# Kernel tuning notes

Hardware: AMD Instinct MI355X
Metric: run time of the kernel (lower is better)

## Reference

```python
import jax, jax.numpy as jnp
import numpy as np

B, T, C = 4, 2048, 1024
H = 16
HD = C // H  # 64
OBS_DIM, ACT_DIM = 17, 6
JOINED_DIM = OBS_DIM + ACT_DIM + 2  # 25


def _make_mask():
    # tril causal mask with every (JOINED_DIM-1 + k*JOINED_DIM)-th column zeroed (RL branch)
    m = np.tril(np.ones((T, T), dtype=np.float32))
    m[:, JOINED_DIM - 1::JOINED_DIM] = 0.0
    return jnp.asarray(m > 0)  # bool [T, T]


MASK = _make_mask()


def setup_inputs() -> dict:
    key = jax.random.key(0)
    ks = jax.random.split(key, 9)
    s = 1.0 / np.sqrt(C)
    return {
        "x": jax.random.normal(ks[0], (B, T, C), dtype=jnp.float32),
        "Wq": jax.random.normal(ks[1], (C, C), dtype=jnp.float32) * s,
        "bq": jax.random.normal(ks[2], (C,), dtype=jnp.float32) * s,
        "Wk": jax.random.normal(ks[3], (C, C), dtype=jnp.float32) * s,
        "bk": jax.random.normal(ks[4], (C,), dtype=jnp.float32) * s,
        "Wv": jax.random.normal(ks[5], (C, C), dtype=jnp.float32) * s,
        "bv": jax.random.normal(ks[6], (C,), dtype=jnp.float32) * s,
        "Wp": jax.random.normal(ks[7], (C, C), dtype=jnp.float32) * s,
        "bp": jax.random.normal(ks[8], (C,), dtype=jnp.float32) * s,
    }


def reference(x, Wq, bq, Wk, bk, Wv, bv, Wp, bp):
    # torch nn.Linear: y = x @ W.T + b
    def split_heads(t):  # [B,T,C] -> [B,H,T,HD]
        return t.reshape(B, T, H, HD).transpose(0, 2, 1, 3)

    q = split_heads(x @ Wq.T + bq)
    k = split_heads(x @ Wk.T + bk)
    v = split_heads(x @ Wv.T + bv)

    att = jnp.einsum("bhqd,bhkd->bhqk", q, k) * (1.0 / np.sqrt(HD))
    att = jnp.where(MASK[None, None, :, :], att, -jnp.inf)
    att = jax.nn.softmax(att, axis=-1)
    # dropout layers are identity in eval mode

    y = jnp.einsum("bhqk,bhkd->bhqd", att, v)  # [B,H,T,HD]
    y = y.transpose(0, 2, 1, 3).reshape(B, T, C)
    return y @ Wp.T + bp
```

## Files before the change

kernel.cpp:

```cpp
#include <hip/hip_runtime.h>
#include <hip/hip_bf16.h>


typedef __attribute__((ext_vector_type(8))) short short8;
typedef __attribute__((ext_vector_type(4))) short short4v;
typedef __attribute__((ext_vector_type(4))) float floatx4;
typedef unsigned short us;

__device__ __forceinline__ us f2bf(float f){
    union { __hip_bfloat16 h; us u; } cv;
    cv.h = __float2bfloat16(f);
    return cv.u;
}

__device__ __forceinline__ void ld_g2l16(const void* g, void* l){
    __builtin_amdgcn_global_load_lds((const __attribute__((address_space(1))) void*)g,
                                     (__attribute__((address_space(3))) void*)l, 16, 0, 0);
}

__global__ __launch_bounds__(256) void cvt_kernel(const float* __restrict__ in,
                                                  us* __restrict__ out, int n4){
    int i = blockIdx.x * 256 + threadIdx.x;
    if (i < n4){
        float4 v = reinterpret_cast<const float4*>(in)[i];
        ushort4 o;
        o.x = f2bf(v.x); o.y = f2bf(v.y); o.z = f2bf(v.z); o.w = f2bf(v.w);
        reinterpret_cast<ushort4*>(out)[i] = o;
    }
}

__global__ __launch_bounds__(256) void cvt4_kernel(const float* __restrict__ w0, const float* __restrict__ w1,
                                                   const float* __restrict__ w2, const float* __restrict__ w3,
                                                   us* __restrict__ o0, us* __restrict__ o1,
                                                   us* __restrict__ o2, us* __restrict__ o3){
    int wsel = blockIdx.x >> 10;
    int i = (blockIdx.x & 1023) * 256 + threadIdx.x;
    const float* src = (wsel == 0) ? w0 : (wsel == 1) ? w1 : (wsel == 2) ? w2 : w3;
    us* dst = (wsel == 0) ? o0 : (wsel == 1) ? o1 : (wsel == 2) ? o2 : o3;
    float4 v = reinterpret_cast<const float4*>(src)[i];
    ushort4 o;
    o.x = f2bf(v.x); o.y = f2bf(v.y); o.z = f2bf(v.z); o.w = f2bf(v.w);
    reinterpret_cast<ushort4*>(dst)[i] = o;
}


#define QSCALE 0.1803368801111244f

#define BAR() __builtin_amdgcn_s_barrier()
#define SGB0() __builtin_amdgcn_sched_barrier(0)
#define LGKM0() do { asm volatile("s_waitcnt lgkmcnt(0)" ::: "memory"); __builtin_amdgcn_sched_barrier(0); } while(0)
#define VMC6() asm volatile("s_waitcnt vmcnt(6)" ::: "memory")
#define VMC4() asm volatile("s_waitcnt vmcnt(4)" ::: "memory")
#define VMC0() asm volatile("s_waitcnt vmcnt(0)" ::: "memory")

#define STAGE_A3(buf, kt) do { \
    _Pragma("unroll") \
    for (int c_ = 0; c_ < 4; c_++) \
        ld_g2l16(Ag + (size_t)(m0 + srow[c_])*1024 + (kt)*64 + sgr[c_]*8, \
                 &smem[(buf)*24576 + (c_*8 + wave)*512]); \
} while(0)

#define STAGE_B3(buf, kt) do { \
    _Pragma("unroll") \
    for (int c_ = 0; c_ < 2; c_++) \
        ld_g2l16(Wb + (size_t)(n0 + srow[c_])*1024 + (kt)*64 + sgr[c_]*8, \
                 &smem[(buf)*24576 + 16384 + (c_*8 + wave)*512]); \
} while(0)

#define LOAD_SET3(buf, KS, AF, BF) do { \
    _Pragma("unroll") \
    for (int i_ = 0; i_ < 4; i_++){ \
        int ra_ = wmm*64 + i_*16 + lane15; \
        int ga_ = ((KS)*4 + quad) ^ (ra_ & 7); \
        AF[i_] = *reinterpret_cast<const short8*>(&smem[(buf)*24576 + ra_*64 + ga_*8]); \
    } \
    _Pragma("unroll") \
    for (int j_ = 0; j_ < 4; j_++){ \
        int rb_ = wnn*64 + j_*16 + lane15; \
        int gb_ = ((KS)*4 + quad) ^ (rb_ & 7); \
        BF[j_] = *reinterpret_cast<const short8*>(&smem[(buf)*24576 + 16384 + rb_*64 + gb_*8]); \
    } \
} while(0)

#define MFMA_SET3(AF, BF) do { \
    __builtin_amdgcn_s_setprio(1); \
    _Pragma("unroll") \
    for (int i_ = 0; i_ < 4; i_++) \
        _Pragma("unroll") \
        for (int j_ = 0; j_ < 4; j_++) \
            acc[i_][j_] = __builtin_amdgcn_mfma_f32_16x16x32_bf16( \
                AF[i_], BF[j_], acc[i_][j_], 0, 0, 0); \
    __builtin_amdgcn_s_setprio(0); \
} while(0)

#define KLOOP3() do { \
    STAGE_A3(0, 0); STAGE_B3(0, 0); \
    STAGE_A3(1, 1); STAGE_B3(1, 1); \
    VMC6(); BAR(); \
    LOAD_SET3(0, 0, afE, bfE); LGKM0(); \
    _Pragma("unroll") \
    for (int t = 0; t < 16; t++){ \
        const int cur = t % 3, nxt = (t + 2) % 3, nx1 = (t + 1) % 3; \
         \
        LOAD_SET3(cur, 1, afO, bfO); \
        SGB0(); \
        if (t < 14) STAGE_A3(nxt, t + 2); \
        MFMA_SET3(afE, bfE); \
        LGKM0(); \
        if (t < 14) { VMC4(); } else if (t == 14) { VMC0(); } \
        BAR(); \
         \
        if (t < 15){ LOAD_SET3(nx1, 0, afE, bfE); SGB0(); } \
        if (t < 14) STAGE_B3(nxt, t + 2); \
        MFMA_SET3(afO, bfO); \
        LGKM0(); \
        BAR(); \
    } \
} while(0)

__global__ __launch_bounds__(512, 2) void gemm_qkv3(
    const us* __restrict__ Ag,
    const us* __restrict__ Wqb, const us* __restrict__ Wkb, const us* __restrict__ Wvb,
    const float* __restrict__ bq, const float* __restrict__ bk, const float* __restrict__ bv,
    us* __restrict__ qo, us* __restrict__ ko, us* __restrict__ vto)
{
    __shared__ us smem[73728];
    const int tid = threadIdx.x;
    const int lane = tid & 63;
    const int wave = tid >> 6;
    const int lane15 = lane & 15;
    const int quad = lane >> 4;
    const int wmm = wave & 3;
    const int wnn = wave >> 2;
    const int seg = blockIdx.x >> 3;
    const int n0 = (blockIdx.x & 7) * 128;
    const int m0 = blockIdx.y * 256;

    const us* Wb = (seg == 0) ? Wqb : (seg == 1) ? Wkb : Wvb;
    const float* bias = (seg == 0) ? bq : (seg == 1) ? bk : bv;

    int srow[4], sgr[4];
    #pragma unroll
    for (int c = 0; c < 4; c++){
        int s = (c*8 + wave)*64 + lane;
        srow[c] = s >> 3;
        sgr[c] = (s & 7) ^ ((s >> 3) & 7);
    }

    floatx4 zero = {0.f, 0.f, 0.f, 0.f};
    floatx4 acc[4][4];
    #pragma unroll
    for (int i = 0; i < 4; i++)
        #pragma unroll
        for (int j = 0; j < 4; j++) acc[i][j] = zero;
    short8 afE[4], bfE[4], afO[4], bfO[4];

    KLOOP3();

    if (seg < 2){
        #pragma unroll
        for (int i = 0; i < 4; i++){
            #pragma unroll
            for (int j = 0; j < 4; j++){
                int n = n0 + wnn*64 + j*16 + lane15;
                float bvv = bias[n];
                #pragma unroll
                for (int r = 0; r < 4; r++){
                    int m = m0 + wmm*64 + i*16 + quad*4 + r;
                    float val = acc[i][j][r] + bvv;
                    if (seg == 0){
                        qo[(size_t)m*1024 + n] = f2bf(val * QSCALE);
                    } else {
                        int b = m >> 11, tt = m & 2047;
                        int h = n >> 6,  d = n & 63;
                        ko[(((size_t)b*16 + h)*2048 + tt)*64 + d] = f2bf(val);
                    }
                }
            }
        }
    } else {
        us* lCT = smem;
        const int b = m0 >> 11;
        const int t0 = m0 & 2047;
        #pragma unroll
        for (int j = 0; j < 4; j++){
            int nl = wnn*64 + j*16 + lane15;
            float bvv = bias[n0 + nl];
            #pragma unroll
            for (int i = 0; i < 4; i++){
                int ml = wmm*64 + i*16 + quad*4;
                unsigned int lo = (unsigned int)f2bf(acc[i][j][0] + bvv) |
                                  ((unsigned int)f2bf(acc[i][j][1] + bvv) << 16);
                unsigned int hi = (unsigned int)f2bf(acc[i][j][2] + bvv) |
                                  ((unsigned int)f2bf(acc[i][j][3] + bvv) << 16);
                uint2 pk2; pk2.x = lo; pk2.y = hi;
                *reinterpret_cast<uint2*>(&lCT[(size_t)nl*264 + ml]) = pk2;
            }
        }
        __syncthreads();
        int nl = tid >> 2;
        int c4 = tid & 3;
        int nC = n0 + nl;
        int h = nC >> 6, d = nC & 63;
        us* dst = vto + (((size_t)b*16 + h)*64 + d)*2048 + t0 + c4*64;
        int rr = (t0 + c4*64) % 25;
        #pragma unroll
        for (int ii = 0; ii < 8; ii++){
            uint4 v = *reinterpret_cast<const uint4*>(&lCT[(size_t)nl*264 + c4*64 + ii*8]);
            us* pv = reinterpret_cast<us*>(&v);
            #pragma unroll
            for (int e = 0; e < 8; e++){
                if (rr == 24) pv[e] = 0;
                rr = (rr == 24) ? 0 : rr + 1;
            }
            *reinterpret_cast<uint4*>(dst + ii*8) = v;
        }
    }
}

__device__ __forceinline__ short8 rdP(const us* pw, int lane15, int ks, int quad){
    const us* a = &pw[lane15*68 + ks*32 + quad*8];
    short4v lo = *reinterpret_cast<const short4v*>(a);
    short4v hi = *reinterpret_cast<const short4v*>(a + 4);
    short8 r = {lo[0], lo[1], lo[2], lo[3], hi[0], hi[1], hi[2], hi[3]};
    return r;
}

__device__ __forceinline__ void pstore_plain(floatx4 (&s)[4], us* pw, int lane15, int quad){
    #pragma unroll
    for (int tj = 0; tj < 4; tj++)
        #pragma unroll
        for (int r = 0; r < 4; r++)
            pw[(quad*4 + r)*68 + tj*16 + lane15] = f2bf(__builtin_amdgcn_exp2f(s[tj][r]));
}

__device__ __forceinline__ void pstore_diag(floatx4 (&s)[4], us* pw, int rgrow, int j0,
                                            int lane15, int quad){
    #pragma unroll
    for (int tj = 0; tj < 4; tj++){
        #pragma unroll
        for (int r = 0; r < 4; r++){
            float p = __builtin_amdgcn_exp2f(s[tj][r]);
            bool kill = (j0 + tj*16 + lane15) > (rgrow + quad*4 + r);
            pw[(quad*4 + r)*68 + tj*16 + lane15] = f2bf(kill ? 0.f : p);
        }
    }
}

#define ATT_STAGE(itn) do { \
    _Pragma("unroll") \
    for (int i_ = 0; i_ < 2; i_++){ \
        ld_g2l16(kb + (size_t)((itn)*64 + srow[i_])*64 + sgr[i_]*8, &lK[(itn) & 1][(i_*4 + wave)*512]); \
        ld_g2l16(vb + (size_t)srow[i_]*2048 + (itn)*64 + sgr[i_]*8, &lV[(itn) & 1][(i_*4 + wave)*512]); \
    } } while(0)

#define ATT_BODY(MODE, ITV) do { \
    const int j0_ = (ITV)*64; \
    __syncthreads(); \
    if ((ITV) + 1 < nIter) ATT_STAGE((ITV) + 1); \
    const us* Kb = lK[(ITV) & 1]; \
    const us* Vb = lV[(ITV) & 1]; \
    floatx4 s0[4], s1[4]; \
    __builtin_amdgcn_s_setprio(1); \
    _Pragma("unroll") \
    for (int tj = 0; tj < 4; tj++){ \
        int rk = tj*16 + lane15; \
        short8 kf0 = *reinterpret_cast<const short8*>(&Kb[rk*64 + ((quad     ^ (rk & 7)))*8]); \
        short8 kf1 = *reinterpret_cast<const short8*>(&Kb[rk*64 + (((4+quad) ^ (rk & 7)))*8]); \
        floatx4 z1 = __builtin_amdgcn_mfma_f32_16x16x32_bf16(qf1a, kf0, zero, 0, 0, 0); \
        s1[tj]     = __builtin_amdgcn_mfma_f32_16x16x32_bf16(qf1b, kf1, z1,   0, 0, 0); \
        if ((MODE) != 2){ \
            floatx4 z0 = __builtin_amdgcn_mfma_f32_16x16x32_bf16(qf0a, kf0, zero, 0, 0, 0); \
            s0[tj]     = __builtin_amdgcn_mfma_f32_16x16x32_bf16(qf0b, kf1, z0,   0, 0, 0); \
        } \
    } \
    __builtin_amdgcn_s_setprio(0); \
    if ((MODE) == 2)      pstore_diag(s1, pw1, rg1, j0_, lane15, quad); \
    else                  pstore_plain(s1, pw1, lane15, quad); \
    if ((MODE) == 1)      pstore_diag(s0, pw0, rg0, j0_, lane15, quad); \
    else if ((MODE) == 0) pstore_plain(s0, pw0, lane15, quad); \
    __builtin_amdgcn_s_setprio(1); \
    _Pragma("unroll") \
    for (int ks = 0; ks < 2; ks++){ \
        short8 mfr = *reinterpret_cast<const short8*>(&lmask[j0_ + ks*32 + quad*8]); \
        short8 pf1 = rdP(pw1, lane15, ks, quad); \
        short8 pf0; \
        lacc1 = __builtin_amdgcn_mfma_f32_16x16x32_bf16(pf1, mfr, lacc1, 0, 0, 0); \
        if ((MODE) != 2){ \
            pf0 = rdP(pw0, lane15, ks, quad); \
            lacc0 = __builtin_amdgcn_mfma_f32_16x16x32_bf16(pf0, mfr, lacc0, 0, 0, 0); \
        } \
        _Pragma("unroll") \
        for (int dt = 0; dt < 4; dt++){ \
            int rv = dt*16 + lane15; \
            short8 vf = *reinterpret_cast<const short8*>(&Vb[rv*64 + (((ks*4+quad) ^ (rv & 7)))*8]); \
            acc1[dt] = __builtin_amdgcn_mfma_f32_16x16x32_bf16(pf1, vf, acc1[dt], 0, 0, 0); \
            if ((MODE) != 2) acc0[dt] = __builtin_amdgcn_mfma_f32_16x16x32_bf16(pf0, vf, acc0[dt], 0, 0, 0); \
        } \
    } \
    __builtin_amdgcn_s_setprio(0); \
} while(0)

__global__ __launch_bounds__(256, 3) void flash_attn(
    const us* __restrict__ q,
    const us* __restrict__ k,
    const us* __restrict__ vT,
    us* __restrict__ y)
{
    __shared__ us lK[2][64*64];
    __shared__ us lV[2][64*64];
    __shared__ us lP[4][2][16*68];
    __shared__ us lmask[2048];
    const int tid = threadIdx.x;
    const int lane = tid & 63;
    const int wave = tid >> 6;
    const int lane15 = lane & 15;
    const int quad = lane >> 4;
    const int lin = blockIdx.x;
    const int qt2 = 15 - (lin >> 6);
    const int bh = lin & 63;
    const int b = bh >> 4, h = bh & 15;
    const int rg0 = qt2*128 + wave*16;
    const int rg1 = rg0 + 64;
    const int nIter = 2*qt2 + 2;

    const us* kb = k  + (size_t)bh*2048*64;
    const us* vb = vT + (size_t)bh*64*2048;

    {
        int c0 = tid * 8;
        int rr = c0 % 25;
        ushort4 mv[2];
        us* pm = reinterpret_cast<us*>(mv);
        #pragma unroll
        for (int e = 0; e < 8; e++){
            pm[e] = (rr == 24) ? (us)0 : (us)0x3F80;
            rr = (rr == 24) ? 0 : rr + 1;
        }
        *reinterpret_cast<uint4*>(&lmask[c0]) = *reinterpret_cast<uint4*>(mv);
    }

    floatx4 zero = {0.f, 0.f, 0.f, 0.f};
    us* pw0 = &lP[wave][0][0];
    us* pw1 = &lP[wave][1][0];

    int srow[2], sgr[2];
    #pragma unroll
    for (int i = 0; i < 2; i++){
        int s = (i*4 + wave)*64 + lane;
        srow[i] = s >> 3;
        sgr[i] = (s & 7) ^ ((s >> 3) & 7);
    }

    const us* q0 = q + ((size_t)b*2048 + rg0 + lane15)*1024 + h*64 + quad*8;
    const us* q1 = q + ((size_t)b*2048 + rg1 + lane15)*1024 + h*64 + quad*8;
    short8 qf0a = *reinterpret_cast<const short8*>(q0);
    short8 qf0b = *reinterpret_cast<const short8*>(q0 + 32);
    short8 qf1a = *reinterpret_cast<const short8*>(q1);
    short8 qf1b = *reinterpret_cast<const short8*>(q1 + 32);

    floatx4 acc0[4], acc1[4];
    #pragma unroll
    for (int d = 0; d < 4; d++){ acc0[d] = zero; acc1[d] = zero; }
    floatx4 lacc0 = zero, lacc1 = zero;

    ATT_STAGE(0);

    int it = 0;
    #pragma unroll 1
    for (; it < nIter - 2; it++) ATT_BODY(0, it);
    ATT_BODY(1, it); it++;
    ATT_BODY(2, it);

    float rl0[4], rl1[4];
    #pragma unroll
    for (int r = 0; r < 4; r++){ rl0[r] = 1.0f / lacc0[r]; rl1[r] = 1.0f / lacc1[r]; }
    #pragma unroll
    for (int dt = 0; dt < 4; dt++){
        #pragma unroll
        for (int r = 0; r < 4; r++){
            int t0 = rg0 + quad*4 + r;
            int t1 = rg1 + quad*4 + r;
            int cc = h*64 + dt*16 + lane15;
            y[((size_t)b*2048 + t0)*1024 + cc] = f2bf(acc0[dt][r] * rl0[r]);
            y[((size_t)b*2048 + t1)*1024 + cc] = f2bf(acc1[dt][r] * rl1[r]);
        }
    }
}

__global__ __launch_bounds__(512, 2) void gemm_out3(
    const us* __restrict__ Ag,
    const us* __restrict__ Wb,
    const float* __restrict__ bias,
    float* __restrict__ out)
{
    __shared__ us smem[73728];
    const int tid = threadIdx.x;
    const int lane = tid & 63;
    const int wave = tid >> 6;
    const int lane15 = lane & 15;
    const int quad = lane >> 4;
    const int wmm = wave & 3;
    const int wnn = wave >> 2;
    const int n0 = blockIdx.x * 128;
    const int m0 = blockIdx.y * 256;

    int srow[4], sgr[4];
    #pragma unroll
    for (int c = 0; c < 4; c++){
        int s = (c*8 + wave)*64 + lane;
        srow[c] = s >> 3;
        sgr[c] = (s & 7) ^ ((s >> 3) & 7);
    }

    floatx4 zero = {0.f, 0.f, 0.f, 0.f};
    floatx4 acc[4][4];
    #pragma unroll
    for (int i = 0; i < 4; i++)
        #pragma unroll
        for (int j = 0; j < 4; j++) acc[i][j] = zero;
    short8 afE[4], bfE[4], afO[4], bfO[4];

    KLOOP3();

    #pragma unroll
    for (int i = 0; i < 4; i++){
        #pragma unroll
        for (int j = 0; j < 4; j++){
            int n = n0 + wnn*64 + j*16 + lane15;
            float bvv = bias[n];
            #pragma unroll
            for (int r = 0; r < 4; r++){
                int m = m0 + wmm*64 + i*16 + quad*4 + r;
                out[(size_t)m*1024 + n] = acc[i][j][r] + bvv;
            }
        }
    }
}

extern "C" void kernel_launch(void* const* d_in, const int* in_sizes, int n_in,
                              void* d_out, int out_size, void* d_ws, size_t ws_size,
                              hipStream_t stream)
{
    const float* x  = (const float*)d_in[0];
    const float* Wq = (const float*)d_in[1];
    const float* bq = (const float*)d_in[2];
    const float* Wk = (const float*)d_in[3];
    const float* bk = (const float*)d_in[4];
    const float* Wv = (const float*)d_in[5];
    const float* bv = (const float*)d_in[6];
    const float* Wp = (const float*)d_in[7];
    const float* bp = (const float*)d_in[8];
    float* out = (float*)d_out;

    us* ws  = (us*)d_ws;
    us* xbf = ws;
    us* wqb = xbf + (size_t)8192*1024;
    us* wkb = wqb + (size_t)1024*1024;
    us* wvb = wkb + (size_t)1024*1024;
    us* wpb = wvb + (size_t)1024*1024;
    us* qws = wpb + (size_t)1024*1024;
    us* kws = qws + (size_t)8388608;
    us* vtw = kws + (size_t)8388608;
    us* yws = vtw + (size_t)8388608;

    cvt_kernel<<<8192, 256, 0, stream>>>(x, xbf, 2097152);
    cvt4_kernel<<<4096, 256, 0, stream>>>(Wq, Wk, Wv, Wp, wqb, wkb, wvb, wpb);

    gemm_qkv3<<<dim3(24, 32), 512, 0, stream>>>(xbf, wqb, wkb, wvb, bq, bk, bv, qws, kws, vtw);

    flash_attn<<<1024, 256, 0, stream>>>(qws, kws, vtw, yws);

    gemm_out3<<<dim3(8, 32), 512, 0, stream>>>(yws, wpb, bp, out);
}
```

Baseline: 256.4 us.

## Enlarge GEMM tiles to 256x256 with double-buffered LDS pipeline

Both projection GEMMs move from 256x128 to 256x256 output tiles, doubling the per-wave accumulator footprint to 4x8 MFMA tiles. The K-loop drops from triple to double buffering with a full vmcnt(0) wait each step, and LDS per block shrinks. The V-transpose epilogue now runs in two passes through shared memory. The aim is more operand reuse per loaded byte, but grids shrink to 384 and 128 blocks, which may underfill 256 CUs. Register pressure grows and overlap of loads with compute is reduced.

```diff
diff --git a/kernel.cpp b/kernel.cpp
--- a/kernel.cpp
+++ b/kernel.cpp
@@ -49,82 +49,76 @@
 #define BAR() __builtin_amdgcn_s_barrier()
 #define SGB0() __builtin_amdgcn_sched_barrier(0)
 #define LGKM0() do { asm volatile("s_waitcnt lgkmcnt(0)" ::: "memory"); __builtin_amdgcn_sched_barrier(0); } while(0)
-#define VMC6() asm volatile("s_waitcnt vmcnt(6)" ::: "memory")
-#define VMC4() asm volatile("s_waitcnt vmcnt(4)" ::: "memory")
 #define VMC0() asm volatile("s_waitcnt vmcnt(0)" ::: "memory")
 
-#define STAGE_A3(buf, kt) do { \
+#define STAGE_A4(buf, kt) do { \
     _Pragma("unroll") \
     for (int c_ = 0; c_ < 4; c_++) \
         ld_g2l16(Ag + (size_t)(m0 + srow[c_])*1024 + (kt)*64 + sgr[c_]*8, \
-                 &smem[(buf)*24576 + (c_*8 + wave)*512]); \
-} while(0)
-
-#define STAGE_B3(buf, kt) do { \
-    _Pragma("unroll") \
-    for (int c_ = 0; c_ < 2; c_++) \
+                 &smem[(buf)*32768 + (c_*8 + wave)*512]); \
+} while(0)
+
+#define STAGE_B4(buf, kt) do { \
+    _Pragma("unroll") \
+    for (int c_ = 0; c_ < 4; c_++) \
         ld_g2l16(Wb + (size_t)(n0 + srow[c_])*1024 + (kt)*64 + sgr[c_]*8, \
-                 &smem[(buf)*24576 + 16384 + (c_*8 + wave)*512]); \
-} while(0)
-
-#define LOAD_SET3(buf, KS, AF, BF) do { \
+                 &smem[(buf)*32768 + 16384 + (c_*8 + wave)*512]); \
+} while(0)
+
+#define LOAD_SET4(buf, KS, AF, BF) do { \
     _Pragma("unroll") \
     for (int i_ = 0; i_ < 4; i_++){ \
         int ra_ = wmm*64 + i_*16 + lane15; \
         int ga_ = ((KS)*4 + quad) ^ (ra_ & 7); \
-        AF[i_] = *reinterpret_cast<const short8*>(&smem[(buf)*24576 + ra_*64 + ga_*8]); \
+        AF[i_] = *reinterpret_cast<const short8*>(&smem[(buf)*32768 + ra_*64 + ga_*8]); \
     } \
     _Pragma("unroll") \
-    for (int j_ = 0; j_ < 4; j_++){ \
-        int rb_ = wnn*64 + j_*16 + lane15; \
+    for (int j_ = 0; j_ < 8; j_++){ \
+        int rb_ = wnn*128 + j_*16 + lane15; \
         int gb_ = ((KS)*4 + quad) ^ (rb_ & 7); \
-        BF[j_] = *reinterpret_cast<const short8*>(&smem[(buf)*24576 + 16384 + rb_*64 + gb_*8]); \
+        BF[j_] = *reinterpret_cast<const short8*>(&smem[(buf)*32768 + 16384 + rb_*64 + gb_*8]); \
     } \
 } while(0)
 
-#define MFMA_SET3(AF, BF) do { \
+#define MFMA_SET4(AF, BF) do { \
     __builtin_amdgcn_s_setprio(1); \
     _Pragma("unroll") \
     for (int i_ = 0; i_ < 4; i_++) \
         _Pragma("unroll") \
-        for (int j_ = 0; j_ < 4; j_++) \
+        for (int j_ = 0; j_ < 8; j_++) \
             acc[i_][j_] = __builtin_amdgcn_mfma_f32_16x16x32_bf16( \
                 AF[i_], BF[j_], acc[i_][j_], 0, 0, 0); \
     __builtin_amdgcn_s_setprio(0); \
 } while(0)
 
-#define KLOOP3() do { \
-    STAGE_A3(0, 0); STAGE_B3(0, 0); \
-    STAGE_A3(1, 1); STAGE_B3(1, 1); \
-    VMC6(); BAR(); \
-    LOAD_SET3(0, 0, afE, bfE); LGKM0(); \
-    _Pragma("unroll") \
+#define KLOOP4() do { \
+    STAGE_A4(0, 0); STAGE_B4(0, 0); \
+    VMC0(); BAR(); \
+    LOAD_SET4(0, 0, afE, bfE); LGKM0(); \
+    _Pragma("unroll 2") \
     for (int t = 0; t < 16; t++){ \
-        const int cur = t % 3, nxt = (t + 2) % 3, nx1 = (t + 1) % 3; \
-         \
-        LOAD_SET3(cur, 1, afO, bfO); \
+        const int cur = t & 1, nxt = cur ^ 1; \
+        LOAD_SET4(cur, 1, afO, bfO); \
         SGB0(); \
-        if (t < 14) STAGE_A3(nxt, t + 2); \
-        MFMA_SET3(afE, bfE); \
+        if (t < 15){ STAGE_A4(nxt, t + 1); STAGE_B4(nxt, t + 1); } \
+        MFMA_SET4(afE, bfE); \
         LGKM0(); \
-        if (t < 14) { VMC4(); } else if (t == 14) { VMC0(); } \
+        if (t < 15) VMC0(); \
         BAR(); \
-         \
-        if (t < 15){ LOAD_SET3(nx1, 0, afE, bfE); SGB0(); } \
-        if (t < 14) STAGE_B3(nxt, t + 2); \
-        MFMA_SET3(afO, bfO); \
+        if (t < 15){ LOAD_SET4(nxt, 0, afE, bfE); SGB0(); } \
+        MFMA_SET4(afO, bfO); \
         LGKM0(); \
         BAR(); \
     } \
 } while(0)
 
-__global__ __launch_bounds__(512, 2) void gemm_qkv3(
+__global__ __launch_bounds__(512, 2) void gemm_qkv4(
     const us* __restrict__ Ag,
     const us* __restrict__ Wqb, const us* __restrict__ Wkb, const us* __restrict__ Wvb,
     const float* __restrict__ bq, const float* __restrict__ bk, const float* __restrict__ bv,
     us* __restrict__ qo, us* __restrict__ ko, us* __restrict__ vto)
 {
-    __shared__ us smem[73728];
+    __shared__ us smem[65536];
     const int tid = threadIdx.x;
     const int lane = tid & 63;
     const int wave = tid >> 6;
@@ -132,8 +126,8 @@
     const int quad = lane >> 4;
     const int wmm = wave & 3;
     const int wnn = wave >> 2;
-    const int seg = blockIdx.x >> 3;
-    const int n0 = (blockIdx.x & 7) * 128;
+    const int seg = blockIdx.x >> 2;
+    const int n0 = (blockIdx.x & 3) * 256;
     const int m0 = blockIdx.y * 256;
 
     const us* Wb = (seg == 0) ? Wqb : (seg == 1) ? Wkb : Wvb;
@@ -148,21 +142,21 @@
     }
 
     floatx4 zero = {0.f, 0.f, 0.f, 0.f};
-    floatx4 acc[4][4];
+    floatx4 acc[4][8];
     #pragma unroll
     for (int i = 0; i < 4; i++)
         #pragma unroll
-        for (int j = 0; j < 4; j++) acc[i][j] = zero;
-    short8 afE[4], bfE[4], afO[4], bfO[4];
-
-    KLOOP3();
+        for (int j = 0; j < 8; j++) acc[i][j] = zero;
+    short8 afE[4], bfE[8], afO[4], bfO[8];
+
+    KLOOP4();
 
     if (seg < 2){
         #pragma unroll
         for (int i = 0; i < 4; i++){
             #pragma unroll
-            for (int j = 0; j < 4; j++){
-                int n = n0 + wnn*64 + j*16 + lane15;
+            for (int j = 0; j < 8; j++){
+                int n = n0 + wnn*128 + j*16 + lane15;
                 float bvv = bias[n];
                 #pragma unroll
                 for (int r = 0; r < 4; r++){
@@ -183,37 +177,43 @@
         const int b = m0 >> 11;
         const int t0 = m0 & 2047;
         #pragma unroll
-        for (int j = 0; j < 4; j++){
-            int nl = wnn*64 + j*16 + lane15;
-            float bvv = bias[n0 + nl];
+        for (int p = 0; p < 2; p++){
+            if (p) __syncthreads();
+            if (wnn == p){
+                #pragma unroll
+                for (int j = 0; j < 8; j++){
+                    int nl = j*16 + lane15;
+                    float bvv = bias[n0 + p*128 + nl];
+                    #pragma unroll
+                    for (int i = 0; i < 4; i++){
+                        int ml = wmm*64 + i*16 + quad*4;
+                        unsigned int lo = (unsigned int)f2bf(acc[i][j][0] + bvv) |
+                                          ((unsigned int)f2bf(acc[i][j][1] + bvv) << 16);
+                        unsigned int hi = (unsigned int)f2bf(acc[i][j][2] + bvv) |
+                                          ((unsigned int)f2bf(acc[i][j][3] + bvv) << 16);
+                        uint2 pk2; pk2.x = lo; pk2.y = hi;
+                        *reinterpret_cast<uint2*>(&lCT[(size_t)nl*264 + ml]) = pk2;
+                    }
+                }
+            }
+            __syncthreads();
+            int nl = tid >> 2;
+            int c4 = tid & 3;
+            int nC = n0 + p*128 + nl;
+            int h = nC >> 6, d = nC & 63;
+            us* dst = vto + (((size_t)b*16 + h)*64 + d)*2048 + t0 + c4*64;
+            int rr = (t0 + c4*64) % 25;
             #pragma unroll
-            for (int i = 0; i < 4; i++){
-                int ml = wmm*64 + i*16 + quad*4;
-                unsigned int lo = (unsigned int)f2bf(acc[i][j][0] + bvv) |
-                                  ((unsigned int)f2bf(acc[i][j][1] + bvv) << 16);
-                unsigned int hi = (unsigned int)f2bf(acc[i][j][2] + bvv) |
-                                  ((unsigned int)f2bf(acc[i][j][3] + bvv) << 16);
-                uint2 pk2; pk2.x = lo; pk2.y = hi;
-                *reinterpret_cast<uint2*>(&lCT[(size_t)nl*264 + ml]) = pk2;
+            for (int ii = 0; ii < 8; ii++){
+                uint4 v = *reinterpret_cast<const uint4*>(&lCT[(size_t)nl*264 + c4*64 + ii*8]);
+                us* pv = reinterpret_cast<us*>(&v);
+                #pragma unroll
+                for (int e = 0; e < 8; e++){
+                    if (rr == 24) pv[e] = 0;
+                    rr = (rr == 24) ? 0 : rr + 1;
+                }
+                *reinterpret_cast<uint4*>(dst + ii*8) = v;
             }
-        }
-        __syncthreads();
-        int nl = tid >> 2;
-        int c4 = tid & 3;
-        int nC = n0 + nl;
-        int h = nC >> 6, d = nC & 63;
-        us* dst = vto + (((size_t)b*16 + h)*64 + d)*2048 + t0 + c4*64;
-        int rr = (t0 + c4*64) % 25;
-        #pragma unroll
-        for (int ii = 0; ii < 8; ii++){
-            uint4 v = *reinterpret_cast<const uint4*>(&lCT[(size_t)nl*264 + c4*64 + ii*8]);
-            us* pv = reinterpret_cast<us*>(&v);
-            #pragma unroll
-            for (int e = 0; e < 8; e++){
-                if (rr == 24) pv[e] = 0;
-                rr = (rr == 24) ? 0 : rr + 1;
-            }
-            *reinterpret_cast<uint4*>(dst + ii*8) = v;
         }
     }
 }
@@ -388,13 +388,13 @@
     }
 }
 
-__global__ __launch_bounds__(512, 2) void gemm_out3(
+__global__ __launch_bounds__(512, 2) void gemm_out4(
     const us* __restrict__ Ag,
     const us* __restrict__ Wb,
     const float* __restrict__ bias,
     float* __restrict__ out)
 {
-    __shared__ us smem[73728];
+    __shared__ us smem[65536];
     const int tid = threadIdx.x;
     const int lane = tid & 63;
     const int wave = tid >> 6;
@@ -402,7 +402,7 @@
     const int quad = lane >> 4;
     const int wmm = wave & 3;
     const int wnn = wave >> 2;
-    const int n0 = blockIdx.x * 128;
+    const int n0 = blockIdx.x * 256;
     const int m0 = blockIdx.y * 256;
 
     int srow[4], sgr[4];
@@ -414,20 +414,20 @@
     }
 
     floatx4 zero = {0.f, 0.f, 0.f, 0.f};
-    floatx4 acc[4][4];
+    floatx4 acc[4][8];
     #pragma unroll
     for (int i = 0; i < 4; i++)
         #pragma unroll
-        for (int j = 0; j < 4; j++) acc[i][j] = zero;
-    short8 afE[4], bfE[4], afO[4], bfO[4];
-
-    KLOOP3();
+        for (int j = 0; j < 8; j++) acc[i][j] = zero;
+    short8 afE[4], bfE[8], afO[4], bfO[8];
+
+    KLOOP4();
 
     #pragma unroll
     for (int i = 0; i < 4; i++){
         #pragma unroll
-        for (int j = 0; j < 4; j++){
-            int n = n0 + wnn*64 + j*16 + lane15;
+        for (int j = 0; j < 8; j++){
+            int n = n0 + wnn*128 + j*16 + lane15;
             float bvv = bias[n];
             #pragma unroll
             for (int r = 0; r < 4; r++){
@@ -467,9 +467,9 @@
     cvt_kernel<<<8192, 256, 0, stream>>>(x, xbf, 2097152);
     cvt4_kernel<<<4096, 256, 0, stream>>>(Wq, Wk, Wv, Wp, wqb, wkb, wvb, wpb);
 
-    gemm_qkv3<<<dim3(24, 32), 512, 0, stream>>>(xbf, wqb, wkb, wvb, bq, bk, bv, qws, kws, vtw);
+    gemm_qkv4<<<dim3(12, 32), 512, 0, stream>>>(xbf, wqb, wkb, wvb, bq, bk, bv, qws, kws, vtw);
 
     flash_attn<<<1024, 256, 0, stream>>>(qws, kws, vtw, yws);
 
-    gemm_out3<<<dim3(8, 32), 512, 0, stream>>>(yws, wpb, bp, out);
-}
+    gemm_out4<<<dim3(4, 32), 512, 0, stream>>>(yws, wpb, bp, out);
+}
```

Result: slower. 660.1 us (+157.4%).
